# Performance work log

Measured on AMD Instinct MI355X. Metric: run time of the kernel, lower is better.

The kernel has to match this reference:

```python
import jax, jax.numpy as jnp
import numpy as np

D_MODEL = 1024
N_HEADS = 16
TOP_FACTOR = 5


def setup_inputs() -> dict:
    key = jax.random.key(0)
    ks = jax.random.split(key, 9)
    B, L, D = 2, 4096, D_MODEL
    s = 0.02
    return {
        "x": jax.random.normal(ks[0], (B, L, D), dtype=jnp.float32),
        "Wq": jax.random.normal(ks[1], (D, D), dtype=jnp.float32) * s,
        "bq": jnp.zeros((D,), dtype=jnp.float32),
        "Wk": jax.random.normal(ks[2], (D, D), dtype=jnp.float32) * s,
        "bk": jnp.zeros((D,), dtype=jnp.float32),
        "Wv": jax.random.normal(ks[3], (D, D), dtype=jnp.float32) * s,
        "bv": jnp.zeros((D,), dtype=jnp.float32),
        "Wo": jax.random.normal(ks[4], (D, D), dtype=jnp.float32) * s,
        "bo": jnp.zeros((D,), dtype=jnp.float32),
    }


def reference(x, Wq, bq, Wk, bk, Wv, bv, Wo, bo):
    B, L, D = x.shape
    H = N_HEADS
    hd = D // H
    BH = B * H
    top_u = max(1, L // TOP_FACTOR)

    def proj(W, b):
        # [B,L,D] -> [B*H, L, hd] (matches view + transpose(1,2) in torch)
        y = x @ W.T + b
        return y.reshape(B, L, H, hd).transpose(0, 2, 1, 3).reshape(BH, L, hd)

    Q = proj(Wq, bq)
    K = proj(Wk, bk)
    V = proj(Wv, bv)

    # select top-u queries per (batch,head) by L2 norm
    query_norms = jnp.linalg.norm(Q, axis=2)              # [BH, L]
    _, top_idx = jax.lax.top_k(query_norms, top_u)        # [BH, top_u]
    Q_sel = jnp.take_along_axis(Q, top_idx[:, :, None], axis=1)  # [BH, u, hd]

    scale = 1.0 / (hd ** 0.5)
    scores = jnp.einsum('bud,bld->bul', Q_sel, K) * scale  # [BH, u, L]
    attn = jax.nn.softmax(scores, axis=-1)
    out_sel = jnp.einsum('bul,bld->bud', attn, V)          # [BH, u, hd]

    # scatter selected outputs back; non-selected rows stay zero
    out_full = jnp.zeros((BH, L, hd), dtype=x.dtype)
    out_full = out_full.at[jnp.arange(BH)[:, None], top_idx].set(out_sel)

    out = out_full.reshape(B, H, L, hd).transpose(0, 2, 1, 3).reshape(B, L, D)
    return out @ Wo.T + bo
```

## Files before the change

kernel.cpp:

```cpp
#include <hip/hip_runtime.h>
#include <cstddef>
#include <cstdint>

constexpr int LSEQ = 4096;
constexpr int DM   = 1024;
constexpr int HD   = 64;
constexpr int BHT  = 32;
constexpr int TOPU = 819;
constexpr int MROWS = 8192;

typedef unsigned short u16;
typedef __attribute__((ext_vector_type(8))) short short8v;
typedef __attribute__((ext_vector_type(4))) short short4v;
typedef __attribute__((ext_vector_type(4))) float f32x4;

__device__ __forceinline__ u16 f2bf(float f) {
  uint32_t u = __float_as_uint(f);
  u += 0x7fffu + ((u >> 16) & 1u);
  return (u16)(u >> 16);
}
__device__ __forceinline__ float bf2f(u16 h) {
  return __uint_as_float(((uint32_t)h) << 16);
}

__device__ __forceinline__ void gl16(const void* g, void* l) {
  __builtin_amdgcn_global_load_lds(
      (const __attribute__((address_space(1))) void*)g,
      (__attribute__((address_space(3))) void*)l, 16, 0, 0);
}

__device__ __forceinline__ void inv_swz(int S, int& R, int& C) {
  const int R0 = ((S >> 5) ^ (S >> 7)) & 1;
  const int R1 = (S >> 6) & 1;
  R = ((S >> 6) << 1) | R0;
  C = (((S >> 3) & 1) ^ R0) | ((((S >> 4) & 1) ^ R1) << 1);
}

__device__ __forceinline__ void split3_body(const float* src, u16* p1, u16* p2,
                                            u16* p3, int i) {
  const float4 a = *reinterpret_cast<const float4*>(src + (size_t)i * 8);
  const float4 b = *reinterpret_cast<const float4*>(src + (size_t)i * 8 + 4);
  float e[8] = {a.x, a.y, a.z, a.w, b.x, b.y, b.z, b.w};
  short8v v1, v2, v3;
  #pragma unroll
  for (int j = 0; j < 8; ++j) {
    u16 h1 = f2bf(e[j]);        float r1 = e[j] - bf2f(h1);
    u16 h2 = f2bf(r1);          float r2 = r1 - bf2f(h2);
    u16 h3 = f2bf(r2);
    v1[j] = (short)h1; v2[j] = (short)h2; v3[j] = (short)h3;
  }
  *reinterpret_cast<short8v*>(p1 + (size_t)i * 8) = v1;
  *reinterpret_cast<short8v*>(p2 + (size_t)i * 8) = v2;
  *reinterpret_cast<short8v*>(p3 + (size_t)i * 8) = v3;
}

__device__ __forceinline__ void conv_body(const float* src, u16* dst, int i) {
  const float4 a = *reinterpret_cast<const float4*>(src + (size_t)i * 8);
  const float4 b = *reinterpret_cast<const float4*>(src + (size_t)i * 8 + 4);
  short8v v;
  v[0] = (short)f2bf(a.x); v[1] = (short)f2bf(a.y);
  v[2] = (short)f2bf(a.z); v[3] = (short)f2bf(a.w);
  v[4] = (short)f2bf(b.x); v[5] = (short)f2bf(b.y);
  v[6] = (short)f2bf(b.z); v[7] = (short)f2bf(b.w);
  *reinterpret_cast<short8v*>(dst + (size_t)i * 8) = v;
}

__global__ __launch_bounds__(256) void prep_all(
    const float* __restrict__ x,  const float* __restrict__ Wq,
    const float* __restrict__ Wk, const float* __restrict__ Wv,
    const float* __restrict__ Wo,
    u16* __restrict__ x1, u16* __restrict__ x2, u16* __restrict__ x3,
    u16* __restrict__ wq1, u16* __restrict__ wq2, u16* __restrict__ wq3,
    u16* __restrict__ Wkb, u16* __restrict__ Wvb, u16* __restrict__ Wob)
{
  const int NX = MROWS * DM / 8;
  const int NW = DM * DM / 8;
  int i = blockIdx.x * 256 + threadIdx.x;
  if (i < NX)  { split3_body(x,  x1,  x2,  x3,  i); return; }
  i -= NX;
  if (i < NW)  { split3_body(Wq, wq1, wq2, wq3, i); return; }
  i -= NW;
  if (i < NW)  { conv_body(Wk, Wkb, i); return; }
  i -= NW;
  if (i < NW)  { conv_body(Wv, Wvb, i); return; }
  i -= NW;
  if (i < NW)  { conv_body(Wo, Wob, i); }
}

__device__ __forceinline__ void proj_q_body(
    u16* smem,
    const u16* __restrict__ X1, const u16* __restrict__ X2, const u16* __restrict__ X3,
    const u16* __restrict__ W1, const u16* __restrict__ W2, const u16* __restrict__ W3,
    const float* __restrict__ bias, float* __restrict__ Y,
    float* __restrict__ norms, int bx, int ny)
{
  u16* As[3] = {smem, smem + 4096, smem + 8192};
  u16* Bs[3] = {smem + 12288, smem + 16384, smem + 20480};
  const int tid = threadIdx.x;
  const int m0 = bx * 128, n0 = ny * 128;
  const int wid = tid >> 6, lane = tid & 63;
  const int wr = (wid >> 1) * 64, wc = (wid & 1) * 64;
  const int c = lane & 15, G = lane >> 4;

  int Rr[2], Cr[2];
  #pragma unroll
  for (int rr = 0; rr < 2; ++rr) inv_swz((tid + rr * 256) * 8, Rr[rr], Cr[rr]);

  f32x4 acc[4][4];
  #pragma unroll
  for (int mt = 0; mt < 4; ++mt)
    #pragma unroll
    for (int nt = 0; nt < 4; ++nt)
      acc[mt][nt] = (f32x4){0.f, 0.f, 0.f, 0.f};

  for (int k0 = 0; k0 < DM; k0 += 32) {
    #pragma unroll
    for (int rr = 0; rr < 2; ++rr) {
      const size_t goA = (size_t)(m0 + Rr[rr]) * DM + k0 + Cr[rr] * 8;
      const size_t goB = (size_t)(n0 + Rr[rr]) * DM + k0 + Cr[rr] * 8;
      const int lb = wid * 512 + rr * 2048;
      gl16(X1 + goA, As[0] + lb);
      gl16(X2 + goA, As[1] + lb);
      gl16(X3 + goA, As[2] + lb);
      gl16(W1 + goB, Bs[0] + lb);
      gl16(W2 + goB, Bs[1] + lb);
      gl16(W3 + goB, Bs[2] + lb);
    }
    __syncthreads();

    short8v bf[3][4];
    #pragma unroll
    for (int nt = 0; nt < 4; ++nt) {
      const int n = wc + nt * 16 + c;
      const int eo = (n * 32 + G * 8) ^ ((n & 7) << 3);
      bf[0][nt] = *reinterpret_cast<const short8v*>(Bs[0] + eo);
      bf[1][nt] = *reinterpret_cast<const short8v*>(Bs[1] + eo);
      bf[2][nt] = *reinterpret_cast<const short8v*>(Bs[2] + eo);
    }
    #pragma unroll
    for (int mt = 0; mt < 4; ++mt) {
      const int m = wr + mt * 16 + c;
      const int eo = (m * 32 + G * 8) ^ ((m & 7) << 3);
      short8v a1 = *reinterpret_cast<const short8v*>(As[0] + eo);
      short8v a2 = *reinterpret_cast<const short8v*>(As[1] + eo);
      short8v a3 = *reinterpret_cast<const short8v*>(As[2] + eo);
      #pragma unroll
      for (int nt = 0; nt < 4; ++nt) {
        acc[mt][nt] = __builtin_amdgcn_mfma_f32_16x16x32_bf16(a1, bf[0][nt], acc[mt][nt], 0, 0, 0);
        acc[mt][nt] = __builtin_amdgcn_mfma_f32_16x16x32_bf16(a1, bf[1][nt], acc[mt][nt], 0, 0, 0);
        acc[mt][nt] = __builtin_amdgcn_mfma_f32_16x16x32_bf16(a2, bf[0][nt], acc[mt][nt], 0, 0, 0);
        acc[mt][nt] = __builtin_amdgcn_mfma_f32_16x16x32_bf16(a2, bf[1][nt], acc[mt][nt], 0, 0, 0);
        acc[mt][nt] = __builtin_amdgcn_mfma_f32_16x16x32_bf16(a1, bf[2][nt], acc[mt][nt], 0, 0, 0);
        acc[mt][nt] = __builtin_amdgcn_mfma_f32_16x16x32_bf16(a3, bf[0][nt], acc[mt][nt], 0, 0, 0);
      }
    }
    __syncthreads();
  }

  float bb[4];
  #pragma unroll
  for (int nt = 0; nt < 4; ++nt) bb[nt] = bias[n0 + wc + nt * 16 + c];

  float ns[4][4];
  #pragma unroll
  for (int mt = 0; mt < 4; ++mt)
    #pragma unroll
    for (int r = 0; r < 4; ++r) ns[mt][r] = 0.f;

  #pragma unroll
  for (int mt = 0; mt < 4; ++mt) {
    #pragma unroll
    for (int nt = 0; nt < 4; ++nt) {
      const int n = n0 + wc + nt * 16 + c;
      const int h = n >> 6, d = n & 63;
      #pragma unroll
      for (int r = 0; r < 4; ++r) {
        const int m = m0 + wr + mt * 16 + G * 4 + r;
        const int b = m >> 12, l = m & (LSEQ - 1);
        const float val = acc[mt][nt][r] + bb[nt];
        Y[((size_t)((b << 4) + h) * LSEQ + l) * HD + d] = val;
        ns[mt][r] = fmaf(val, val, ns[mt][r]);
      }
    }
  }
  #pragma unroll
  for (int mt = 0; mt < 4; ++mt)
    #pragma unroll
    for (int r = 0; r < 4; ++r) {
      float v = ns[mt][r];
      v += __shfl_xor(v, 1); v += __shfl_xor(v, 2);
      v += __shfl_xor(v, 4); v += __shfl_xor(v, 8);
      ns[mt][r] = v;
    }
  if (c == 0) {
    const int h = (n0 + wc) >> 6;
    #pragma unroll
    for (int mt = 0; mt < 4; ++mt)
      #pragma unroll
      for (int r = 0; r < 4; ++r) {
        const int m = m0 + wr + mt * 16 + G * 4 + r;
        const int b = m >> 12, l = m & (LSEQ - 1);
        norms[(((size_t)((b << 4) + h)) << 12) + l] = ns[mt][r];
      }
  }
}

__device__ __forceinline__ void proj_kv_body(
    u16* smem, const u16* __restrict__ Xb, const u16* __restrict__ Wb,
    const float* __restrict__ bias, u16* __restrict__ Kb, u16* __restrict__ VgT,
    bool isV, int bx, int ny)
{
  u16* As = smem;
  u16* Bs = smem + 4096;
  const int tid = threadIdx.x;
  const int m0 = bx * 128, n0 = ny * 128;
  const int wid = tid >> 6, lane = tid & 63;
  const int wr = (wid >> 1) * 64, wc = (wid & 1) * 64;
  const int c = lane & 15, G = lane >> 4;

  int Rr[2], Cr[2];
  #pragma unroll
  for (int rr = 0; rr < 2; ++rr) inv_swz((tid + rr * 256) * 8, Rr[rr], Cr[rr]);

  f32x4 acc[4][4];
  #pragma unroll
  for (int mt = 0; mt < 4; ++mt)
    #pragma unroll
    for (int nt = 0; nt < 4; ++nt)
      acc[mt][nt] = (f32x4){0.f, 0.f, 0.f, 0.f};

  for (int k0 = 0; k0 < DM; k0 += 32) {
    #pragma unroll
    for (int rr = 0; rr < 2; ++rr) {
      const size_t goA = (size_t)(m0 + Rr[rr]) * DM + k0 + Cr[rr] * 8;
      const size_t goB = (size_t)(n0 + Rr[rr]) * DM + k0 + Cr[rr] * 8;
      const int lb = wid * 512 + rr * 2048;
      gl16(Xb + goA, As + lb);
      gl16(Wb + goB, Bs + lb);
    }
    __syncthreads();

    short8v af[4], bf[4];
    #pragma unroll
    for (int mt = 0; mt < 4; ++mt) {
      const int m = wr + mt * 16 + c;
      af[mt] = *reinterpret_cast<const short8v*>(As + ((m * 32 + G * 8) ^ ((m & 7) << 3)));
      const int n = wc + mt * 16 + c;
      bf[mt] = *reinterpret_cast<const short8v*>(Bs + ((n * 32 + G * 8) ^ ((n & 7) << 3)));
    }
    #pragma unroll
    for (int mt = 0; mt < 4; ++mt)
      #pragma unroll
      for (int nt = 0; nt < 4; ++nt)
        acc[mt][nt] = __builtin_amdgcn_mfma_f32_16x16x32_bf16(af[mt], bf[nt], acc[mt][nt], 0, 0, 0);
    __syncthreads();
  }

  float bb[4];
  #pragma unroll
  for (int nt = 0; nt < 4; ++nt) bb[nt] = bias[n0 + wc + nt * 16 + c];

  if (isV) {
    #pragma unroll
    for (int mt = 0; mt < 4; ++mt) {
      #pragma unroll
      for (int nt = 0; nt < 4; ++nt) {
        const int n = wc + nt * 16 + c;
        const int mloc = wr + mt * 16 + G * 4;
        short4v pv;
        #pragma unroll
        for (int r = 0; r < 4; ++r) pv[r] = (short)f2bf(acc[mt][nt][r] + bb[nt]);
        *reinterpret_cast<short4v*>(smem + n * 136 + mloc) = pv;
      }
    }
    __syncthreads();
    const int bb2 = m0 >> 12;
    const int ml0 = m0 & (LSEQ - 1);
    #pragma unroll
    for (int uu = 0; uu < 8; ++uu) {
      const int u = uu * 256 + tid;
      const int n = u >> 4, kg = u & 15;
      short8v vvv = *reinterpret_cast<const short8v*>(smem + n * 136 + kg * 8);
      const int h = (n0 + n) >> 6, d = (n0 + n) & 63;
      *reinterpret_cast<short8v*>(
          VgT + ((size_t)((bb2 << 4) + h) * HD + d) * LSEQ + ml0 + kg * 8) = vvv;
    }
  } else {
    #pragma unroll
    for (int mt = 0; mt < 4; ++mt) {
      #pragma unroll
      for (int nt = 0; nt < 4; ++nt) {
        const int n = n0 + wc + nt * 16 + c;
        const int h = n >> 6, d = n & 63;
        #pragma unroll
        for (int r = 0; r < 4; ++r) {
          const int m = m0 + wr + mt * 16 + G * 4 + r;
          const int b = m >> 12, l = m & (LSEQ - 1);
          Kb[((size_t)((b << 4) + h) * LSEQ + l) * HD + d] = f2bf(acc[mt][nt][r] + bb[nt]);
        }
      }
    }
  }
}

__global__ __launch_bounds__(256) void gemm_proj(
    const u16* __restrict__ X1, const u16* __restrict__ X2, const u16* __restrict__ X3,
    const u16* __restrict__ W1, const u16* __restrict__ W2, const u16* __restrict__ W3,
    const u16* __restrict__ Wkb, const u16* __restrict__ Wvb,
    const float* __restrict__ bq, const float* __restrict__ bk, const float* __restrict__ bv,
    float* __restrict__ Qb, float* __restrict__ norms,
    u16* __restrict__ Kb, u16* __restrict__ VgT, int y_off)
{
  __shared__ u16 smem[24576];
  const int by = blockIdx.y + y_off;
  const int bx = blockIdx.x;
  if (by < 8) {
    proj_q_body(smem, X1, X2, X3, W1, W2, W3, bq, Qb, norms, bx, by);
  } else if (by < 16) {
    proj_kv_body(smem, X1, Wvb, bv, Kb, VgT, true, bx, by - 8);
  } else {
    proj_kv_body(smem, X1, Wkb, bk, Kb, VgT, false, bx, by - 16);
  }
}

__global__ __launch_bounds__(256) void gemm_out(
    const u16* __restrict__ Xb, const u16* __restrict__ Wb,
    const float* __restrict__ bias, float* __restrict__ Y)
{
  __shared__ u16 As[128 * 32];
  __shared__ u16 Bs[128 * 32];
  const int tid = threadIdx.x;
  const int m0 = blockIdx.x * 128, n0 = blockIdx.y * 128;
  const int wid = tid >> 6, lane = tid & 63;
  const int wr = (wid >> 1) * 64, wc = (wid & 1) * 64;
  const int c = lane & 15, G = lane >> 4;

  int Rr[2], Cr[2];
  #pragma unroll
  for (int rr = 0; rr < 2; ++rr) inv_swz((tid + rr * 256) * 8, Rr[rr], Cr[rr]);

  f32x4 acc[4][4];
  #pragma unroll
  for (int mt = 0; mt < 4; ++mt)
    #pragma unroll
    for (int nt = 0; nt < 4; ++nt)
      acc[mt][nt] = (f32x4){0.f, 0.f, 0.f, 0.f};

  for (int k0 = 0; k0 < DM; k0 += 32) {
    #pragma unroll
    for (int rr = 0; rr < 2; ++rr) {
      const size_t goA = (size_t)(m0 + Rr[rr]) * DM + k0 + Cr[rr] * 8;
      const size_t goB = (size_t)(n0 + Rr[rr]) * DM + k0 + Cr[rr] * 8;
      const int lb = wid * 512 + rr * 2048;
      gl16(Xb + goA, As + lb);
      gl16(Wb + goB, Bs + lb);
    }
    __syncthreads();

    short8v af[4], bf[4];
    #pragma unroll
    for (int mt = 0; mt < 4; ++mt) {
      const int m = wr + mt * 16 + c;
      af[mt] = *reinterpret_cast<const short8v*>(As + ((m * 32 + G * 8) ^ ((m & 7) << 3)));
      const int n = wc + mt * 16 + c;
      bf[mt] = *reinterpret_cast<const short8v*>(Bs + ((n * 32 + G * 8) ^ ((n & 7) << 3)));
    }
    #pragma unroll
    for (int mt = 0; mt < 4; ++mt)
      #pragma unroll
      for (int nt = 0; nt < 4; ++nt)
        acc[mt][nt] = __builtin_amdgcn_mfma_f32_16x16x32_bf16(af[mt], bf[nt], acc[mt][nt], 0, 0, 0);
    __syncthreads();
  }

  float bb[4];
  #pragma unroll
  for (int nt = 0; nt < 4; ++nt) bb[nt] = bias[n0 + wc + nt * 16 + c];

  #pragma unroll
  for (int mt = 0; mt < 4; ++mt) {
    #pragma unroll
    for (int nt = 0; nt < 4; ++nt) {
      const int n = n0 + wc + nt * 16 + c;
      #pragma unroll
      for (int r = 0; r < 4; ++r) {
        const int m = m0 + wr + mt * 16 + G * 4 + r;
        Y[(size_t)m * DM + n] = acc[mt][nt][r] + bb[nt];
      }
    }
  }
}

__global__ __launch_bounds__(1024) void select_topk(
    const float* __restrict__ norms, int* __restrict__ top_idx)
{
  __shared__ unsigned int keys[LSEQ];
  __shared__ unsigned int hist[256];
  __shared__ unsigned int wsums[16];
  __shared__ unsigned int sh_b, sh_above;

  const int tid = threadIdx.x;
  const int bh = blockIdx.x;

  for (int l = tid; l < LSEQ; l += 1024)
    keys[l] = __float_as_uint(norms[bh * LSEQ + l]);
  __syncthreads();

  unsigned int prefix = 0, rem = TOPU, total_gt = 0;
  for (int shift = 24; shift >= 0; shift -= 8) {
    if (tid < 256) hist[tid] = 0;
    __syncthreads();
    for (int l = tid; l < LSEQ; l += 1024) {
      const unsigned int k = keys[l];
      const bool in = (shift == 24) || ((k >> (shift + 8)) == prefix);
      if (in) atomicAdd(&hist[(k >> shift) & 255], 1);
    }
    __syncthreads();
    if (tid == 0) {
      unsigned int cum = 0; int b = 255;
      for (; b > 0; --b) {
        const unsigned int h = hist[b];
        if (cum + h >= rem) break;
        cum += h;
      }
      sh_b = (unsigned int)b; sh_above = cum;
    }
    __syncthreads();
    prefix = (prefix << 8) | sh_b;
    total_gt += sh_above;
    rem -= sh_above;
    __syncthreads();
  }
  const unsigned int T = prefix;

  const int lane = tid & 63, wv = tid >> 6;
  const int l0 = tid * 4;

  {
    unsigned int flags = 0; int cnt = 0;
    #pragma unroll
    for (int j = 0; j < 4; ++j)
      if (keys[l0 + j] > T) { flags |= 1u << j; ++cnt; }
    int incl = cnt;
    #pragma unroll
    for (int off = 1; off < 64; off <<= 1) {
      int nv = __shfl_up(incl, off);
      if (lane >= off) incl += nv;
    }
    if (lane == 63) wsums[wv] = (unsigned int)incl;
    __syncthreads();
    if (tid == 0) {
      unsigned int run = 0;
      for (int w = 0; w < 16; ++w) { unsigned int t = wsums[w]; wsums[w] = run; run += t; }
    }
    __syncthreads();
    unsigned int pos = wsums[wv] + (unsigned int)(incl - cnt);
    #pragma unroll
    for (int j = 0; j < 4; ++j)
      if (flags & (1u << j)) top_idx[bh * TOPU + (pos++)] = l0 + j;
  }
  __syncthreads();

  {
    unsigned int flags = 0; int cnt = 0;
    #pragma unroll
    for (int j = 0; j < 4; ++j)
      if (keys[l0 + j] == T) { flags |= 1u << j; ++cnt; }
    int incl = cnt;
    #pragma unroll
    for (int off = 1; off < 64; off <<= 1) {
      int nv = __shfl_up(incl, off);
      if (lane >= off) incl += nv;
    }
    if (lane == 63) wsums[wv] = (unsigned int)incl;
    __syncthreads();
    if (tid == 0) {
      unsigned int run = 0;
      for (int w = 0; w < 16; ++w) { unsigned int t = wsums[w]; wsums[w] = run; run += t; }
    }
    __syncthreads();
    unsigned int r0 = wsums[wv] + (unsigned int)(incl - cnt);
    #pragma unroll
    for (int j = 0; j < 4; ++j)
      if (flags & (1u << j)) {
        if (r0 < rem) top_idx[bh * TOPU + total_gt + r0] = l0 + j;
        ++r0;
      }
  }
}

__global__ __launch_bounds__(256) void attn_mfma(
    const float* __restrict__ Qf, const u16* __restrict__ Kg,
    const u16* __restrict__ VgT, const int* __restrict__ tix,
    float* __restrict__ Opart, float* __restrict__ MLpart)
{
  __shared__ u16 Kc[128 * 64];
  __shared__ u16 Vt[64 * 128];
  __shared__ u16 Pt[4][16 * 136];

  const int tid = threadIdx.x;
  const int wid = tid >> 6, lane = tid & 63;
  const int c = lane & 15, G = lane >> 4;

  const int l = blockIdx.x;
  const int grp = l >> 3;
  const int bh = (grp / 26) * 8 + (l & 7);
  const int rem = grp % 26;
  const int qb = rem >> 1, ks = rem & 1;

  const size_t bhL = (size_t)bh * LSEQ;
  const int rglob = qb * 64 + wid * 16 + c;
  const int rowidx = (rglob < TOPU) ? tix[bh * TOPU + rglob] : -1;

  short8v qf[2];
  #pragma unroll
  for (int kf = 0; kf < 2; ++kf) {
    if (rowidx >= 0) {
      const float* qp = Qf + (bhL + rowidx) * HD + kf * 32 + G * 8;
      const float4 x0 = *reinterpret_cast<const float4*>(qp);
      const float4 x1 = *reinterpret_cast<const float4*>(qp + 4);
      short8v v;
      v[0] = (short)f2bf(x0.x * 0.125f); v[1] = (short)f2bf(x0.y * 0.125f);
      v[2] = (short)f2bf(x0.z * 0.125f); v[3] = (short)f2bf(x0.w * 0.125f);
      v[4] = (short)f2bf(x1.x * 0.125f); v[5] = (short)f2bf(x1.y * 0.125f);
      v[6] = (short)f2bf(x1.z * 0.125f); v[7] = (short)f2bf(x1.w * 0.125f);
      qf[kf] = v;
    } else {
      short8v v;
      #pragma unroll
      for (int j = 0; j < 8; ++j) v[j] = 0;
      qf[kf] = v;
    }
  }

  float m = -1e30f, lsum = 0.f;
  f32x4 oacc[4];
  #pragma unroll
  for (int dt = 0; dt < 4; ++dt) oacc[dt] = (f32x4){0.f, 0.f, 0.f, 0.f};

  const int ko0 = ks * (LSEQ / 2);
  const int wbase = (tid & ~63) * 8;
  for (int t = 0; t < LSEQ / 256; ++t) {
    const int ko = ko0 + t * 128;
    #pragma unroll
    for (int uu = 0; uu < 4; ++uu) {
      const int S = (uu * 256 + tid) * 8;
      const int key = S >> 6, dgk = ((S >> 3) & 7) ^ (key & 7);
      gl16(Kg + (bhL + ko + key) * HD + dgk * 8, Kc + uu * 2048 + wbase);
      const int d = S >> 7, kgv = ((S >> 3) & 15) ^ (d & 7);
      gl16(VgT + ((size_t)bh * HD + d) * LSEQ + ko + kgv * 8, Vt + uu * 2048 + wbase);
    }
    __syncthreads();

    f32x4 sacc[8];
    __builtin_amdgcn_s_setprio(1);
    #pragma unroll
    for (int kt = 0; kt < 8; ++kt) {
      const int key = kt * 16 + c;
      short8v kb0 = *reinterpret_cast<const short8v*>(
          Kc + key * 64 + (((0 + G) ^ (key & 7)) << 3));
      short8v kb1 = *reinterpret_cast<const short8v*>(
          Kc + key * 64 + (((4 + G) ^ (key & 7)) << 3));
      f32x4 s = (f32x4){0.f, 0.f, 0.f, 0.f};
      s = __builtin_amdgcn_mfma_f32_16x16x32_bf16(kb0, qf[0], s, 0, 0, 0);
      s = __builtin_amdgcn_mfma_f32_16x16x32_bf16(kb1, qf[1], s, 0, 0, 0);
      sacc[kt] = s;
    }
    __builtin_amdgcn_s_setprio(0);

    float smax = -1e30f;
    #pragma unroll
    for (int kt = 0; kt < 8; ++kt) {
      float a0 = fmaxf(sacc[kt][0], sacc[kt][1]);
      float a1 = fmaxf(sacc[kt][2], sacc[kt][3]);
      smax = fmaxf(smax, fmaxf(a0, a1));
    }
    smax = fmaxf(smax, __shfl_xor(smax, 16));
    smax = fmaxf(smax, __shfl_xor(smax, 32));
    const float mnew = fmaxf(m, smax);
    const float corr = __expf(m - mnew);
    float ssum = 0.f;
    #pragma unroll
    for (int kt = 0; kt < 8; ++kt) {
      float p0 = __expf(sacc[kt][0] - mnew);
      float p1 = __expf(sacc[kt][1] - mnew);
      float p2 = __expf(sacc[kt][2] - mnew);
      float p3 = __expf(sacc[kt][3] - mnew);
      ssum += (p0 + p1) + (p2 + p3);
      short4v pv;
      pv[0] = (short)f2bf(p0); pv[1] = (short)f2bf(p1);
      pv[2] = (short)f2bf(p2); pv[3] = (short)f2bf(p3);
      *reinterpret_cast<short4v*>(&Pt[wid][c * 136 + kt * 16 + G * 4]) = pv;
    }
    ssum += __shfl_xor(ssum, 16);
    ssum += __shfl_xor(ssum, 32);
    lsum = lsum * corr + ssum;
    m = mnew;
    #pragma unroll
    for (int dt = 0; dt < 4; ++dt) oacc[dt] *= corr;

    __builtin_amdgcn_s_setprio(1);
    #pragma unroll
    for (int kf = 0; kf < 4; ++kf) {
      short8v pf = *reinterpret_cast<const short8v*>(
          &Pt[wid][c * 136 + kf * 32 + G * 8]);
      #pragma unroll
      for (int dt = 0; dt < 4; ++dt) {
        const int d = dt * 16 + c;
        short8v vf = *reinterpret_cast<const short8v*>(
            Vt + d * 128 + (((kf * 4 + G) ^ (d & 7)) << 3));
        oacc[dt] = __builtin_amdgcn_mfma_f32_16x16x32_bf16(vf, pf, oacc[dt], 0, 0, 0);
      }
    }
    __builtin_amdgcn_s_setprio(0);
    __syncthreads();
  }

  const int q = wid * 16 + c;
  const size_t pb = ((size_t)(bh * 13 + qb) * 2 + ks) * 64 + q;
  float* op = Opart + pb * 64;
  #pragma unroll
  for (int dt = 0; dt < 4; ++dt)
    *reinterpret_cast<f32x4*>(op + dt * 16 + G * 4) = oacc[dt];
  if (G == 0) {
    MLpart[pb * 2]     = m;
    MLpart[pb * 2 + 1] = lsum;
  }
}

__global__ __launch_bounds__(256) void attn_combine(
    const float* __restrict__ Opart, const float* __restrict__ MLpart,
    const int* __restrict__ tix, u16* __restrict__ O1b)
{
  const int bq = blockIdx.x;
  const int bh = bq / 13, qb = bq % 13;
  const int tid = threadIdx.x;
  const int q = tid >> 2, dq = (tid & 3) * 16;
  const int rglob = qb * 64 + q;
  if (rglob >= TOPU) return;
  const int rowidx = tix[bh * TOPU + rglob];

  const size_t p0 = ((size_t)bq * 2 + 0) * 64 + q;
  const size_t p1 = ((size_t)bq * 2 + 1) * 64 + q;
  const float m0 = MLpart[p0 * 2], l0 = MLpart[p0 * 2 + 1];
  const float m1 = MLpart[p1 * 2], l1 = MLpart[p1 * 2 + 1];
  const float mx = fmaxf(m0, m1);
  const float c0 = __expf(m0 - mx), c1 = __expf(m1 - mx);
  const float linv = 1.0f / (l0 * c0 + l1 * c1);

  const int b = bh >> 4, h = bh & 15;
  u16* dst = O1b + (size_t)(b * LSEQ + rowidx) * DM + h * HD + dq;
  const float* o0 = Opart + p0 * 64 + dq;
  const float* o1 = Opart + p1 * 64 + dq;
  #pragma unroll
  for (int i = 0; i < 16; i += 4) {
    float4 a  = *reinterpret_cast<const float4*>(o0 + i);
    float4 bb = *reinterpret_cast<const float4*>(o1 + i);
    short4v o;
    o[0] = (short)f2bf((a.x * c0 + bb.x * c1) * linv);
    o[1] = (short)f2bf((a.y * c0 + bb.y * c1) * linv);
    o[2] = (short)f2bf((a.z * c0 + bb.z * c1) * linv);
    o[3] = (short)f2bf((a.w * c0 + bb.w * c1) * linv);
    *reinterpret_cast<short4v*>(dst + i) = o;
  }
}

extern "C" void kernel_launch(void* const* d_in, const int* in_sizes, int n_in,
                              void* d_out, int out_size, void* d_ws, size_t ws_size,
                              hipStream_t stream) {
  const float* x  = (const float*)d_in[0];
  const float* Wq = (const float*)d_in[1];
  const float* bq = (const float*)d_in[2];
  const float* Wk = (const float*)d_in[3];
  const float* bk = (const float*)d_in[4];
  const float* Wv = (const float*)d_in[5];
  const float* bv = (const float*)d_in[6];
  const float* Wo = (const float*)d_in[7];
  const float* bo = (const float*)d_in[8];
  float* out = (float*)d_out;

  char* w = (char*)d_ws;
  float* Qb = (float*)w;  w += (size_t)BHT * LSEQ * HD * 4;
  u16* x1   = (u16*)w;    w += (size_t)MROWS * DM * 2;
  u16* x2   = (u16*)w;    w += (size_t)MROWS * DM * 2;
  u16* x3   = (u16*)w;    w += (size_t)MROWS * DM * 2;
  u16* VgT  = (u16*)w;    w += (size_t)BHT * HD * LSEQ * 2;
  u16* Wkb  = (u16*)w;    w += (size_t)DM * DM * 2;
  u16* Wvb  = (u16*)w;    w += (size_t)DM * DM * 2;
  u16* Wob  = (u16*)w;    w += (size_t)DM * DM * 2;
  u16* wq1  = (u16*)w;    w += (size_t)DM * DM * 2;
  u16* wq2  = (u16*)w;    w += (size_t)DM * DM * 2;
  u16* wq3  = (u16*)w;    w += (size_t)DM * DM * 2;
  float* norms = (float*)w; w += (size_t)BHT * LSEQ * 4;
  u16* Kb_ext = (u16*)w;  w += (size_t)BHT * LSEQ * HD * 2;

  const bool fusedK = ws_size >= (size_t)(w - (char*)d_ws);
  u16* Kb = fusedK ? Kb_ext : x3;

  u16*   O1b  = x2;
  int*   tix  = (int*)wq2;
  float* Opart  = (float*)x1;
  float* MLpart = Opart + (size_t)832 * 64 * 64;

  prep_all<<<6144, 256, 0, stream>>>(x, Wq, Wk, Wv, Wo,
                                     x1, x2, x3, wq1, wq2, wq3, Wkb, Wvb, Wob);

  if (fusedK) {
    gemm_proj<<<dim3(64, 24), 256, 0, stream>>>(
        x1, x2, x3, wq1, wq2, wq3, Wkb, Wvb, bq, bk, bv, Qb, norms, Kb, VgT, 0);
  } else {
    gemm_proj<<<dim3(64, 16), 256, 0, stream>>>(
        x1, x2, x3, wq1, wq2, wq3, Wkb, Wvb, bq, bk, bv, Qb, norms, Kb, VgT, 0);
    gemm_proj<<<dim3(64, 8), 256, 0, stream>>>(
        x1, x2, x3, wq1, wq2, wq3, Wkb, Wvb, bq, bk, bv, Qb, norms, Kb, VgT, 16);
  }

  select_topk<<<BHT, 1024, 0, stream>>>(norms, tix);

  hipMemsetAsync(O1b, 0, (size_t)MROWS * DM * 2, stream);

  attn_mfma<<<832, 256, 0, stream>>>(Qb, Kb, VgT, tix, Opart, MLpart);
  attn_combine<<<416, 256, 0, stream>>>(Opart, MLpart, tix, O1b);

  gemm_out<<<dim3(MROWS / 128, DM / 128), 256, 0, stream>>>(O1b, Wob, bo, out);
}
```

Before: 297.0 us.

## Split attention keys into four segments and store partial outputs in bf16

The attention kernel now splits each query block's key range into four segments instead of two, doubling the grid to 1664 blocks with half as many iterations each. This gives the GPU more blocks to spread across its compute units. Partial outputs are stored as bf16 instead of fp32 to cut the write and read traffic between the attention and combine kernels. The combine kernel merges four partials with a log-sum-exp rescale, which adds reduction work and some rounding error from the bf16 partials.

After: 287.3 us. -3.3%, faster.

```diff
diff --git a/kernel.cpp b/kernel.cpp
--- a/kernel.cpp
+++ b/kernel.cpp
@@ -8,6 +8,7 @@
 constexpr int BHT  = 32;
 constexpr int TOPU = 819;
 constexpr int MROWS = 8192;
+constexpr int NSEG = 4;
 
 typedef unsigned short u16;
 typedef __attribute__((ext_vector_type(8))) short short8v;
@@ -311,7 +312,7 @@
     float* __restrict__ Qb, float* __restrict__ norms,
     u16* __restrict__ Kb, u16* __restrict__ VgT, int y_off)
 {
-  __shared__ u16 smem[24576];
+  __shared__ __align__(16) u16 smem[24576];
   const int by = blockIdx.y + y_off;
   const int bx = blockIdx.x;
   if (by < 8) {
@@ -492,7 +493,7 @@
 __global__ __launch_bounds__(256) void attn_mfma(
     const float* __restrict__ Qf, const u16* __restrict__ Kg,
     const u16* __restrict__ VgT, const int* __restrict__ tix,
-    float* __restrict__ Opart, float* __restrict__ MLpart)
+    u16* __restrict__ OpartB, float* __restrict__ MLpart)
 {
   __shared__ u16 Kc[128 * 64];
   __shared__ u16 Vt[64 * 128];
@@ -504,9 +505,9 @@
 
   const int l = blockIdx.x;
   const int grp = l >> 3;
-  const int bh = (grp / 26) * 8 + (l & 7);
-  const int rem = grp % 26;
-  const int qb = rem >> 1, ks = rem & 1;
+  const int bh = (grp / 52) * 8 + (l & 7);
+  const int rem = grp % 52;
+  const int qb = rem >> 2, ks = rem & 3;
 
   const size_t bhL = (size_t)bh * LSEQ;
   const int rglob = qb * 64 + wid * 16 + c;
@@ -538,9 +539,9 @@
   #pragma unroll
   for (int dt = 0; dt < 4; ++dt) oacc[dt] = (f32x4){0.f, 0.f, 0.f, 0.f};
 
-  const int ko0 = ks * (LSEQ / 2);
+  const int ko0 = ks * (LSEQ / NSEG);
   const int wbase = (tid & ~63) * 8;
-  for (int t = 0; t < LSEQ / 256; ++t) {
+  for (int t = 0; t < LSEQ / NSEG / 128; ++t) {
     const int ko = ko0 + t * 128;
     #pragma unroll
     for (int uu = 0; uu < 4; ++uu) {
@@ -617,11 +618,15 @@
   }
 
   const int q = wid * 16 + c;
-  const size_t pb = ((size_t)(bh * 13 + qb) * 2 + ks) * 64 + q;
-  float* op = Opart + pb * 64;
-  #pragma unroll
-  for (int dt = 0; dt < 4; ++dt)
-    *reinterpret_cast<f32x4*>(op + dt * 16 + G * 4) = oacc[dt];
+  const size_t pb = ((size_t)((bh * 13 + qb) * NSEG + ks)) * 64 + q;
+  u16* op = OpartB + pb * 64;
+  #pragma unroll
+  for (int dt = 0; dt < 4; ++dt) {
+    short4v o;
+    o[0] = (short)f2bf(oacc[dt][0]); o[1] = (short)f2bf(oacc[dt][1]);
+    o[2] = (short)f2bf(oacc[dt][2]); o[3] = (short)f2bf(oacc[dt][3]);
+    *reinterpret_cast<short4v*>(op + dt * 16 + G * 4) = o;
+  }
   if (G == 0) {
     MLpart[pb * 2]     = m;
     MLpart[pb * 2 + 1] = lsum;
@@ -629,7 +634,7 @@
 }
 
 __global__ __launch_bounds__(256) void attn_combine(
-    const float* __restrict__ Opart, const float* __restrict__ MLpart,
+    const u16* __restrict__ OpartB, const float* __restrict__ MLpart,
     const int* __restrict__ tix, u16* __restrict__ O1b)
 {
   const int bq = blockIdx.x;
@@ -640,28 +645,38 @@
   if (rglob >= TOPU) return;
   const int rowidx = tix[bh * TOPU + rglob];
 
-  const size_t p0 = ((size_t)bq * 2 + 0) * 64 + q;
-  const size_t p1 = ((size_t)bq * 2 + 1) * 64 + q;
-  const float m0 = MLpart[p0 * 2], l0 = MLpart[p0 * 2 + 1];
-  const float m1 = MLpart[p1 * 2], l1 = MLpart[p1 * 2 + 1];
-  const float mx = fmaxf(m0, m1);
-  const float c0 = __expf(m0 - mx), c1 = __expf(m1 - mx);
-  const float linv = 1.0f / (l0 * c0 + l1 * c1);
+  size_t p[NSEG];
+  float mi[NSEG], li[NSEG];
+  #pragma unroll
+  for (int i = 0; i < NSEG; ++i) {
+    p[i] = ((size_t)bq * NSEG + i) * 64 + q;
+    mi[i] = MLpart[p[i] * 2];
+    li[i] = MLpart[p[i] * 2 + 1];
+  }
+  float mx = fmaxf(fmaxf(mi[0], mi[1]), fmaxf(mi[2], mi[3]));
+  float ci[NSEG], lsum = 0.f;
+  #pragma unroll
+  for (int i = 0; i < NSEG; ++i) { ci[i] = __expf(mi[i] - mx); lsum += li[i] * ci[i]; }
+  const float linv = 1.0f / lsum;
+
+  float acc[16];
+  #pragma unroll
+  for (int j = 0; j < 16; ++j) acc[j] = 0.f;
+  #pragma unroll
+  for (int i = 0; i < NSEG; ++i) {
+    const u16* src = OpartB + p[i] * 64 + dq;
+    #pragma unroll
+    for (int j = 0; j < 16; ++j) acc[j] += bf2f(src[j]) * ci[i];
+  }
 
   const int b = bh >> 4, h = bh & 15;
   u16* dst = O1b + (size_t)(b * LSEQ + rowidx) * DM + h * HD + dq;
-  const float* o0 = Opart + p0 * 64 + dq;
-  const float* o1 = Opart + p1 * 64 + dq;
-  #pragma unroll
-  for (int i = 0; i < 16; i += 4) {
-    float4 a  = *reinterpret_cast<const float4*>(o0 + i);
-    float4 bb = *reinterpret_cast<const float4*>(o1 + i);
+  #pragma unroll
+  for (int j0 = 0; j0 < 16; j0 += 4) {
     short4v o;
-    o[0] = (short)f2bf((a.x * c0 + bb.x * c1) * linv);
-    o[1] = (short)f2bf((a.y * c0 + bb.y * c1) * linv);
-    o[2] = (short)f2bf((a.z * c0 + bb.z * c1) * linv);
-    o[3] = (short)f2bf((a.w * c0 + bb.w * c1) * linv);
-    *reinterpret_cast<short4v*>(dst + i) = o;
+    #pragma unroll
+    for (int j = 0; j < 4; ++j) o[j] = (short)f2bf(acc[j0 + j] * linv);
+    *reinterpret_cast<short4v*>(dst + j0) = o;
   }
 }
 
@@ -697,10 +712,11 @@
   const bool fusedK = ws_size >= (size_t)(w - (char*)d_ws);
   u16* Kb = fusedK ? Kb_ext : x3;
 
-  u16*   O1b  = x2;
-  int*   tix  = (int*)wq2;
-  float* Opart  = (float*)x1;
-  float* MLpart = Opart + (size_t)832 * 64 * 64;
+  u16*   O1b    = x2;
+  int*   tix    = (int*)wq2;
+  u16*   OpartB = x1;
+  const int NPB = BHT * 13 * NSEG * 64;
+  float* MLpart = (float*)(OpartB + (size_t)NPB * 64);
 
   prep_all<<<6144, 256, 0, stream>>>(x, Wq, Wk, Wv, Wo,
                                      x1, x2, x3, wq1, wq2, wq3, Wkb, Wvb, Wob);
@@ -719,8 +735,8 @@
 
   hipMemsetAsync(O1b, 0, (size_t)MROWS * DM * 2, stream);
 
-  attn_mfma<<<832, 256, 0, stream>>>(Qb, Kb, VgT, tix, Opart, MLpart);
-  attn_combine<<<416, 256, 0, stream>>>(Opart, MLpart, tix, O1b);
+  attn_mfma<<<BHT * 13 * NSEG, 256, 0, stream>>>(Qb, Kb, VgT, tix, OpartB, MLpart);
+  attn_combine<<<BHT * 13, 256, 0, stream>>>(OpartB, MLpart, tix, O1b);
 
   gemm_out<<<dim3(MROWS / 128, DM / 128), 256, 0, stream>>>(O1b, Wob, bo, out);
 }
```
